# Performance work log

Hardware: AMD Instinct MI355X
Metric: run time of the kernel (lower is better)

## Reference

```python
import jax, jax.numpy as jnp
import numpy as np

LORA_ALPHA = 16.0

def setup_inputs() -> dict:
    key = jax.random.key(0)
    kx, kw, ka, kb, kbias = jax.random.split(key, 5)
    B_, S, D_in, D_out, R = 2, 4096, 4096, 4096, 16
    x = jax.random.normal(kx, (B_, S, D_in), dtype=jnp.float32)
    W = jax.random.normal(kw, (D_out, D_in), dtype=jnp.float32) * 0.02
    A = jax.random.normal(ka, (R, D_in), dtype=jnp.float32) * 0.02
    Bm = jax.random.normal(kb, (D_out, R), dtype=jnp.float32) * 0.02
    bias = jax.random.normal(kbias, (D_out,), dtype=jnp.float32) * 0.02
    return {"x": x, "W": W, "A": A, "B": Bm, "bias": bias}

def reference(x, W, A, B, bias):
    # y = x @ W.T + bias + (alpha/rank) * (x @ A.T) @ B.T   (dropout p=0)
    rank = A.shape[0]
    lora_scale = LORA_ALPHA / rank
    y = jnp.einsum('bsd,nd->bsn', x, W) + bias
    h = jnp.einsum('bsd,rd->bsr', x, A)          # [B,S,r] low-rank down-proj
    y = y + lora_scale * jnp.einsum('bsr,nr->bsn', h, B)
    return y
```

## Files before the change

### kernel.cpp

```cpp
#include <hip/hip_runtime.h>
#include <hip/hip_bf16.h>

typedef short bf16x8 __attribute__((ext_vector_type(8)));
typedef float f32x4 __attribute__((ext_vector_type(4)));
typedef unsigned short ushort8v __attribute__((ext_vector_type(8)));

__device__ __forceinline__ unsigned short f2bf(float f) {
  unsigned u = __builtin_bit_cast(unsigned, f);
  u += 0x7fffu + ((u >> 16) & 1u);
  return (unsigned short)(u >> 16);
}

__device__ __forceinline__ void gload_lds16(const unsigned short* g, unsigned short* l) {
  __builtin_amdgcn_global_load_lds((const __attribute__((address_space(1))) void*)g,
                                   (__attribute__((address_space(3))) void*)l, 16, 0, 0);
}

__global__ __launch_bounds__(256) void prep_kernel(const float* __restrict__ x,
                                                   const float* __restrict__ W,
                                                   const float* __restrict__ A,
                                                   const float* __restrict__ Bm,
                                                   unsigned short* __restrict__ xb,
                                                   unsigned short* __restrict__ wb,
                                                   float scale, int K, int R, int n8, int t8) {
  int i = blockIdx.x * 256 + threadIdx.x;
  if (i < n8) {
    const float4* p = (const float4*)x + (size_t)i * 2;
    float4 a = p[0], b = p[1];
    ushort8v v;
    v[0] = f2bf(a.x); v[1] = f2bf(a.y); v[2] = f2bf(a.z); v[3] = f2bf(a.w);
    v[4] = f2bf(b.x); v[5] = f2bf(b.y); v[6] = f2bf(b.z); v[7] = f2bf(b.w);
    *((ushort8v*)xb + i) = v;
    return;
  }
  int idx = i - n8;
  if (idx >= t8) return;
  int perRow = K >> 3;
  int n = idx / perRow;
  int d0 = (idx - n * perRow) << 3;
  const float4* wp = (const float4*)(W + (size_t)n * K + d0);
  float4 w0 = wp[0], w1 = wp[1];
  float acc[8] = {w0.x, w0.y, w0.z, w0.w, w1.x, w1.y, w1.z, w1.w};
#pragma unroll 4
  for (int r = 0; r < R; ++r) {
    float c = Bm[(size_t)n * R + r] * scale;
    const float4* ap = (const float4*)(A + (size_t)r * K + d0);
    float4 a0 = ap[0], a1 = ap[1];
    acc[0] += c * a0.x; acc[1] += c * a0.y; acc[2] += c * a0.z; acc[3] += c * a0.w;
    acc[4] += c * a1.x; acc[5] += c * a1.y; acc[6] += c * a1.z; acc[7] += c * a1.w;
  }
  ushort8v v;
#pragma unroll
  for (int j = 0; j < 8; ++j) v[j] = f2bf(acc[j]);
  *((ushort8v*)wb + idx) = v;
}

__global__ __launch_bounds__(256, 2) void gemm_bt_bias_mb(const unsigned short* __restrict__ Xb,
                                                          const unsigned short* __restrict__ Wb,
                                                          const float* __restrict__ bias,
                                                          float* __restrict__ C,
                                                          int M, int N, int K) {
  __shared__ __align__(16) char lds[49152];
  const int t = threadIdx.x;
  const int wave = t >> 6, lane = t & 63;
  const int fr = lane & 15, kc = lane >> 4;
  const int wr = wave >> 1, wc = wave & 1;

  const int NTn = N >> 7;
  const int nwg = gridDim.x;
  int bid = blockIdx.x;
  if ((nwg & 7) == 0) bid = (bid & 7) * (nwg >> 3) + (bid >> 3);
  const int tm = bid / NTn, tn = bid % NTn;
  const int m0 = tm << 8, n0 = tn << 7;

  const int srow = t >> 3;
  const int gch8 = ((t & 7) ^ (srow & 7)) << 3;
  const unsigned short* pa = Xb + (size_t)(m0 + srow) * K + gch8;
  const unsigned short* pb = Wb + (size_t)(n0 + srow) * K + gch8;

  const int swz = (fr & 7) << 4;
  int offA0[8], offB0[4];
#pragma unroll
  for (int m = 0; m < 8; ++m)
    offA0[m] = (wr * 128 + m * 16 + fr) * 128 + ((kc << 4) ^ swz);
#pragma unroll
  for (int n = 0; n < 4; ++n)
    offB0[n] = 32768 + (wc * 64 + n * 16 + fr) * 128 + ((kc << 4) ^ swz);

  f32x4 acc[8][4];
#pragma unroll
  for (int m = 0; m < 8; ++m)
#pragma unroll
    for (int n = 0; n < 4; ++n) acc[m][n] = (f32x4){0.f, 0.f, 0.f, 0.f};

  const size_t K32 = (size_t)32 * K;

  for (int k0 = 0; k0 < K; k0 += 64) {
#pragma unroll
    for (int j = 0; j < 8; ++j)
      gload_lds16(pa + (size_t)j * K32 + k0,
                  (unsigned short*)((char*)lds + j * 4096) + t * 8);
#pragma unroll
    for (int j = 0; j < 4; ++j)
      gload_lds16(pb + (size_t)j * K32 + k0,
                  (unsigned short*)((char*)lds + 32768 + j * 4096) + t * 8);
    __syncthreads();

    bf16x8 af[8], bf[4];
#pragma unroll
    for (int m = 0; m < 8; ++m) af[m] = *(const bf16x8*)((char*)lds + offA0[m]);
#pragma unroll
    for (int n = 0; n < 4; ++n) bf[n] = *(const bf16x8*)((char*)lds + offB0[n]);
#pragma unroll
    for (int m = 0; m < 8; ++m)
#pragma unroll
      for (int n = 0; n < 4; ++n)
        acc[m][n] = __builtin_amdgcn_mfma_f32_16x16x32_bf16(af[m], bf[n], acc[m][n], 0, 0, 0);
#pragma unroll
    for (int m = 0; m < 8; ++m) af[m] = *(const bf16x8*)((char*)lds + (offA0[m] ^ 64));
#pragma unroll
    for (int n = 0; n < 4; ++n) bf[n] = *(const bf16x8*)((char*)lds + (offB0[n] ^ 64));
#pragma unroll
    for (int m = 0; m < 8; ++m)
#pragma unroll
      for (int n = 0; n < 4; ++n)
        acc[m][n] = __builtin_amdgcn_mfma_f32_16x16x32_bf16(af[m], bf[n], acc[m][n], 0, 0, 0);

    __syncthreads();
  }

  const int crow = (lane >> 4) * 4;
  const int ccol = lane & 15;
#pragma unroll
  for (int n = 0; n < 4; ++n) {
    int col = n0 + wc * 64 + n * 16 + ccol;
    float bv = bias[col];
#pragma unroll
    for (int m = 0; m < 8; ++m) {
      int row = m0 + wr * 128 + m * 16 + crow;
      float* cp = C + (size_t)row * N + col;
#pragma unroll
      for (int r = 0; r < 4; ++r) cp[(size_t)r * N] = acc[m][n][r] + bv;
    }
  }
}

__global__ __launch_bounds__(256) void gemm_bt_bias(const unsigned short* __restrict__ Xb,
                                                    const unsigned short* __restrict__ Wb,
                                                    const float* __restrict__ bias,
                                                    float* __restrict__ C,
                                                    int M, int N, int K) {
  __shared__ unsigned short sA[128 * 32];
  __shared__ unsigned short sB[128 * 32];
  const int t = threadIdx.x;
  const int wave = t >> 6, lane = t & 63;
  const int NT = N >> 7;
  const int nwg = gridDim.x;
  int bid = blockIdx.x;
  if ((nwg & 7) == 0) bid = (bid & 7) * (nwg >> 3) + (bid >> 3);
  const int tm = bid / NT, tn = bid % NT;
  const int m0 = tm << 7, n0 = tn << 7;
  const int wr = wave >> 1, wc = wave & 1;

  f32x4 acc[4][4];
#pragma unroll
  for (int m = 0; m < 4; ++m)
#pragma unroll
    for (int n = 0; n < 4; ++n) acc[m][n] = (f32x4){0.f, 0.f, 0.f, 0.f};

  const unsigned short* gA0 = Xb + (size_t)(m0 + (t >> 2)) * K + (t & 3) * 8;
  const unsigned short* gA1 = Xb + (size_t)(m0 + 64 + (t >> 2)) * K + (t & 3) * 8;
  const unsigned short* gB0 = Wb + (size_t)(n0 + (t >> 2)) * K + (t & 3) * 8;
  const unsigned short* gB1 = Wb + (size_t)(n0 + 64 + (t >> 2)) * K + (t & 3) * 8;
  unsigned short* lA0 = sA + (size_t)(wave * 64) * 8;
  unsigned short* lA1 = sA + (size_t)(256 + wave * 64) * 8;
  unsigned short* lB0 = sB + (size_t)(wave * 64) * 8;
  unsigned short* lB1 = sB + (size_t)(256 + wave * 64) * 8;

  const int rrow = lane & 15;
  const int rk = (lane >> 4) * 8;

  for (int k0 = 0; k0 < K; k0 += 32) {
    gload_lds16(gA0 + k0, lA0);
    gload_lds16(gA1 + k0, lA1);
    gload_lds16(gB0 + k0, lB0);
    gload_lds16(gB1 + k0, lB1);
    __syncthreads();
    bf16x8 af[4], bfr[4];
#pragma unroll
    for (int m = 0; m < 4; ++m)
      af[m] = *(const bf16x8*)&sA[(size_t)(wr * 64 + m * 16 + rrow) * 32 + rk];
#pragma unroll
    for (int n = 0; n < 4; ++n)
      bfr[n] = *(const bf16x8*)&sB[(size_t)(wc * 64 + n * 16 + rrow) * 32 + rk];
#pragma unroll
    for (int m = 0; m < 4; ++m)
#pragma unroll
      for (int n = 0; n < 4; ++n)
        acc[m][n] = __builtin_amdgcn_mfma_f32_16x16x32_bf16(af[m], bfr[n], acc[m][n], 0, 0, 0);
    __syncthreads();
  }
  const int crow0 = (lane >> 4) * 4;
  const int ccol = lane & 15;
#pragma unroll
  for (int n = 0; n < 4; ++n) {
    int col = n0 + wc * 64 + n * 16 + ccol;
    float bv = bias[col];
#pragma unroll
    for (int m = 0; m < 4; ++m) {
      int row = m0 + wr * 64 + m * 16 + crow0;
      float* cp = C + (size_t)row * N + col;
#pragma unroll
      for (int r = 0; r < 4; ++r) cp[(size_t)r * N] = acc[m][n][r] + bv;
    }
  }
}

__global__ __launch_bounds__(64) void lora_h_kernel(const float* __restrict__ x,
                                                    const float* __restrict__ A,
                                                    float* __restrict__ h,
                                                    float scale, int K, int R) {
  int m = blockIdx.x, lane = threadIdx.x;
  float acc[16];
#pragma unroll
  for (int r = 0; r < 16; ++r) acc[r] = 0.f;
  for (int d = lane; d < K; d += 64) {
    float xv = x[(size_t)m * K + d];
    for (int r = 0; r < R; ++r) acc[r] += xv * A[(size_t)r * K + d];
  }
  for (int off = 32; off; off >>= 1)
    for (int r = 0; r < R; ++r) acc[r] += __shfl_down(acc[r], off);
  if (lane == 0)
    for (int r = 0; r < R; ++r) h[(size_t)m * R + r] = acc[r] * scale;
}

__global__ __launch_bounds__(256) void fgemm_fallback(const float* __restrict__ X,
                                                      const float* __restrict__ W,
                                                      const float* __restrict__ Bm,
                                                      const float* __restrict__ bias,
                                                      const float* __restrict__ h,
                                                      float* __restrict__ C,
                                                      int M, int N, int K, int R) {
  __shared__ float sX[64][20];
  __shared__ float sW[64][20];
  int nt = N >> 6;
  int bx = blockIdx.x % nt, by = blockIdx.x / nt;
  int m0 = by << 6, n0 = bx << 6;
  int t = threadIdx.x;
  int tx = t & 15, ty = t >> 4;
  float acc[4][4] = {};
  int lrr = t >> 2, lc = (t & 3) << 2;
  for (int k0 = 0; k0 < K; k0 += 16) {
    *(float4*)&sX[lrr][lc] = *(const float4*)&X[(size_t)(m0 + lrr) * K + k0 + lc];
    *(float4*)&sW[lrr][lc] = *(const float4*)&W[(size_t)(n0 + lrr) * K + k0 + lc];
    __syncthreads();
#pragma unroll
    for (int kk = 0; kk < 16; ++kk) {
      float a[4], b[4];
#pragma unroll
      for (int i = 0; i < 4; ++i) a[i] = sX[ty * 4 + i][kk];
#pragma unroll
      for (int j = 0; j < 4; ++j) b[j] = sW[tx * 4 + j][kk];
#pragma unroll
      for (int i = 0; i < 4; ++i)
#pragma unroll
        for (int j = 0; j < 4; ++j) acc[i][j] += a[i] * b[j];
    }
    __syncthreads();
  }
#pragma unroll
  for (int i = 0; i < 4; ++i) {
    int row = m0 + ty * 4 + i;
#pragma unroll
    for (int j = 0; j < 4; ++j) {
      int col = n0 + tx * 4 + j;
      float lo = 0.f;
      for (int r = 0; r < R; ++r) lo += h[(size_t)row * R + r] * Bm[(size_t)col * R + r];
      C[(size_t)row * N + col] = acc[i][j] + bias[col] + lo;
    }
  }
}

extern "C" void kernel_launch(void* const* d_in, const int* in_sizes, int n_in,
                              void* d_out, int out_size, void* d_ws, size_t ws_size,
                              hipStream_t stream) {
  const float* x    = (const float*)d_in[0];
  const float* W    = (const float*)d_in[1];
  const float* A    = (const float*)d_in[2];
  const float* Bm   = (const float*)d_in[3];
  const float* bias = (const float*)d_in[4];
  float* out = (float*)d_out;

  const int N = in_sizes[4];
  const int R = in_sizes[3] / N;
  const int K = in_sizes[2] / R;
  const int M = in_sizes[0] / K;
  const float scale = 16.0f / (float)R;

  const size_t xbytes = (size_t)M * K * 2;
  const size_t wbytes = (size_t)N * K * 2;
  const bool ws_ok = (ws_size >= xbytes + wbytes);
  const bool fastMB  = ws_ok && (M % 256 == 0) && (N % 128 == 0) && (K % 64 == 0) && (K >= 64);
  const bool fast128 = ws_ok && (M % 128 == 0) && (N % 128 == 0) && (K % 32 == 0);

  if (fastMB || fast128) {
    unsigned short* xb = (unsigned short*)d_ws;
    unsigned short* wb = (unsigned short*)((char*)d_ws + xbytes);
    int n8 = M * K / 8;
    int t8 = N * K / 8;
    int total = n8 + t8;
    prep_kernel<<<dim3((total + 255) / 256), dim3(256), 0, stream>>>(x, W, A, Bm, xb, wb,
                                                                     scale, K, R, n8, t8);
    if (fastMB) {
      int grid = (M / 256) * (N / 128);
      gemm_bt_bias_mb<<<dim3(grid), dim3(256), 0, stream>>>(xb, wb, bias, out, M, N, K);
    } else {
      int grid = (M / 128) * (N / 128);
      gemm_bt_bias<<<dim3(grid), dim3(256), 0, stream>>>(xb, wb, bias, out, M, N, K);
    }
  } else {
    float* h = (float*)d_ws;
    lora_h_kernel<<<dim3(M), dim3(64), 0, stream>>>(x, A, h, scale, K, R);
    int grid = (M / 64) * (N / 64);
    fgemm_fallback<<<dim3(grid), dim3(256), 0, stream>>>(x, W, Bm, bias, h, out, M, N, K, R);
  }
}
```

Baseline: 354.8 us.

## Replace 256x128 GEMM with double-buffered 256x256 tile and staged prefetch pipeline

Replaces the single-buffered 256x128 bf16 GEMM with a 256x256 tile that double-buffers K-slices in 128 KB of LDS. Global-to-LDS loads for the next slice are issued in quarters, interleaved with four MFMA quadrant phases under explicit vmcnt waits, barriers and raised wave priority. This targets the exposed load latency of the old per-iteration sync loop and raises arithmetic intensity per loaded byte. The cost is one workgroup per CU, very high register pressure from a 64-entry accumulator array, and a grid of only 256 blocks, which may fill the CUs unevenly.

After: 460.2 us. 1.3x slower.

```diff
diff --git a/kernel.cpp b/kernel.cpp
--- a/kernel.cpp
+++ b/kernel.cpp
@@ -4,6 +4,10 @@
 typedef short bf16x8 __attribute__((ext_vector_type(8)));
 typedef float f32x4 __attribute__((ext_vector_type(4)));
 typedef unsigned short ushort8v __attribute__((ext_vector_type(8)));
+
+#define SBAR() asm volatile("s_barrier" ::: "memory")
+#define SB0() __builtin_amdgcn_sched_barrier(0)
+#define LGKM0() do { asm volatile("s_waitcnt lgkmcnt(0)" ::: "memory"); SB0(); } while (0)
 
 __device__ __forceinline__ unsigned short f2bf(float f) {
   unsigned u = __builtin_bit_cast(unsigned, f);
@@ -55,94 +59,151 @@
   *((ushort8v*)wb + idx) = v;
 }
 
-__global__ __launch_bounds__(256, 2) void gemm_bt_bias_mb(const unsigned short* __restrict__ Xb,
-                                                          const unsigned short* __restrict__ Wb,
-                                                          const float* __restrict__ bias,
-                                                          float* __restrict__ C,
-                                                          int M, int N, int K) {
-  __shared__ __align__(16) char lds[49152];
+__global__ __launch_bounds__(256, 1) void gemm256x4_bt_bias(const unsigned short* __restrict__ Xb,
+                                                            const unsigned short* __restrict__ Wb,
+                                                            const float* __restrict__ bias,
+                                                            float* __restrict__ C,
+                                                            int M, int N, int K) {
+  __shared__ __align__(16) char lds[131072];
   const int t = threadIdx.x;
   const int wave = t >> 6, lane = t & 63;
   const int fr = lane & 15, kc = lane >> 4;
   const int wr = wave >> 1, wc = wave & 1;
 
-  const int NTn = N >> 7;
+  const int NTn = N >> 8;
   const int nwg = gridDim.x;
   int bid = blockIdx.x;
   if ((nwg & 7) == 0) bid = (bid & 7) * (nwg >> 3) + (bid >> 3);
   const int tm = bid / NTn, tn = bid % NTn;
-  const int m0 = tm << 8, n0 = tn << 7;
-
-  const int srow = t >> 3;
-  const int gch8 = ((t & 7) ^ (srow & 7)) << 3;
-  const unsigned short* pa = Xb + (size_t)(m0 + srow) * K + gch8;
-  const unsigned short* pb = Wb + (size_t)(n0 + srow) * K + gch8;
+  const int m0 = tm << 8, n0 = tn << 8;
+
+  const int grow = t >> 3;
+  const int gch8 = ((t & 7) ^ (grow & 7)) << 3;
+  const unsigned short* pa0 = Xb + (size_t)(m0 + grow) * K + gch8;
+  const unsigned short* pb0 = Wb + (size_t)(n0 + grow) * K + gch8;
+  const size_t K32 = (size_t)32 * K;
+  const int sdst = t * 16;
 
   const int swz = (fr & 7) << 4;
-  int offA0[8], offB0[4];
+  const int cb0 = (kc << 4) ^ swz;
+  const int cb1 = ((4 + kc) << 4) ^ swz;
+  const char* rA0[2] = { (char*)lds + wr * 8192 + fr * 128 + cb0,
+                         (char*)lds + 65536 + wr * 8192 + fr * 128 + cb0 };
+  const char* rA1[2] = { (char*)lds + wr * 8192 + fr * 128 + cb1,
+                         (char*)lds + 65536 + wr * 8192 + fr * 128 + cb1 };
+  const char* rB0[2] = { (char*)lds + 32768 + wc * 8192 + fr * 128 + cb0,
+                         (char*)lds + 98304 + wc * 8192 + fr * 128 + cb0 };
+  const char* rB1[2] = { (char*)lds + 32768 + wc * 8192 + fr * 128 + cb1,
+                         (char*)lds + 98304 + wc * 8192 + fr * 128 + cb1 };
+
+  f32x4 acc[8][8];
 #pragma unroll
   for (int m = 0; m < 8; ++m)
-    offA0[m] = (wr * 128 + m * 16 + fr) * 128 + ((kc << 4) ^ swz);
-#pragma unroll
-  for (int n = 0; n < 4; ++n)
-    offB0[n] = 32768 + (wc * 64 + n * 16 + fr) * 128 + ((kc << 4) ^ swz);
-
-  f32x4 acc[8][4];
-#pragma unroll
-  for (int m = 0; m < 8; ++m)
-#pragma unroll
-    for (int n = 0; n < 4; ++n) acc[m][n] = (f32x4){0.f, 0.f, 0.f, 0.f};
-
-  const size_t K32 = (size_t)32 * K;
-
-  for (int k0 = 0; k0 < K; k0 += 64) {
-#pragma unroll
-    for (int j = 0; j < 8; ++j)
-      gload_lds16(pa + (size_t)j * K32 + k0,
-                  (unsigned short*)((char*)lds + j * 4096) + t * 8);
-#pragma unroll
-    for (int j = 0; j < 4; ++j)
-      gload_lds16(pb + (size_t)j * K32 + k0,
-                  (unsigned short*)((char*)lds + 32768 + j * 4096) + t * 8);
-    __syncthreads();
-
-    bf16x8 af[8], bf[4];
-#pragma unroll
-    for (int m = 0; m < 8; ++m) af[m] = *(const bf16x8*)((char*)lds + offA0[m]);
-#pragma unroll
-    for (int n = 0; n < 4; ++n) bf[n] = *(const bf16x8*)((char*)lds + offB0[n]);
-#pragma unroll
-    for (int m = 0; m < 8; ++m)
-#pragma unroll
-      for (int n = 0; n < 4; ++n)
-        acc[m][n] = __builtin_amdgcn_mfma_f32_16x16x32_bf16(af[m], bf[n], acc[m][n], 0, 0, 0);
-#pragma unroll
-    for (int m = 0; m < 8; ++m) af[m] = *(const bf16x8*)((char*)lds + (offA0[m] ^ 64));
-#pragma unroll
-    for (int n = 0; n < 4; ++n) bf[n] = *(const bf16x8*)((char*)lds + (offB0[n] ^ 64));
-#pragma unroll
-    for (int m = 0; m < 8; ++m)
-#pragma unroll
-      for (int n = 0; n < 4; ++n)
-        acc[m][n] = __builtin_amdgcn_mfma_f32_16x16x32_bf16(af[m], bf[n], acc[m][n], 0, 0, 0);
-
-    __syncthreads();
-  }
+#pragma unroll
+    for (int n = 0; n < 8; ++n) acc[m][n] = (f32x4){0.f, 0.f, 0.f, 0.f};
+
+  bf16x8 aF[8], bF0[8], bF1[8];
+
+#define GL(PSRC, DOFF) gload_lds16((PSRC), (unsigned short*)((char*)lds + (DOFF) + sdst))
+#define STG_A01(BUF, COL) do { GL(pa0 + (COL), (BUF)*65536 + 0); \
+    GL(pa0 + K32 + (COL), (BUF)*65536 + 4096); \
+    GL(pa0 + 4*K32 + (COL), (BUF)*65536 + 8192); \
+    GL(pa0 + 5*K32 + (COL), (BUF)*65536 + 12288); } while (0)
+#define STG_A23(BUF, COL) do { GL(pa0 + 2*K32 + (COL), (BUF)*65536 + 16384); \
+    GL(pa0 + 3*K32 + (COL), (BUF)*65536 + 20480); \
+    GL(pa0 + 6*K32 + (COL), (BUF)*65536 + 24576); \
+    GL(pa0 + 7*K32 + (COL), (BUF)*65536 + 28672); } while (0)
+#define STG_B01(BUF, COL) do { GL(pb0 + (COL), (BUF)*65536 + 32768); \
+    GL(pb0 + K32 + (COL), (BUF)*65536 + 36864); \
+    GL(pb0 + 4*K32 + (COL), (BUF)*65536 + 40960); \
+    GL(pb0 + 5*K32 + (COL), (BUF)*65536 + 45056); } while (0)
+#define STG_B23(BUF, COL) do { GL(pb0 + 2*K32 + (COL), (BUF)*65536 + 49152); \
+    GL(pb0 + 3*K32 + (COL), (BUF)*65536 + 53248); \
+    GL(pb0 + 6*K32 + (COL), (BUF)*65536 + 57344); \
+    GL(pb0 + 7*K32 + (COL), (BUF)*65536 + 61440); } while (0)
+
+#define RD_A(BUF, QM) do { \
+    const char* p0_ = rA0[BUF] + (QM)*16384; const char* p1_ = rA1[BUF] + (QM)*16384; \
+    aF[0]=*(const bf16x8*)(p0_);      aF[1]=*(const bf16x8*)(p1_); \
+    aF[2]=*(const bf16x8*)(p0_+2048); aF[3]=*(const bf16x8*)(p1_+2048); \
+    aF[4]=*(const bf16x8*)(p0_+4096); aF[5]=*(const bf16x8*)(p1_+4096); \
+    aF[6]=*(const bf16x8*)(p0_+6144); aF[7]=*(const bf16x8*)(p1_+6144); } while (0)
+#define RD_B(BUF, QN, DST) do { \
+    const char* p0_ = rB0[BUF] + (QN)*16384; const char* p1_ = rB1[BUF] + (QN)*16384; \
+    DST[0]=*(const bf16x8*)(p0_);      DST[1]=*(const bf16x8*)(p1_); \
+    DST[2]=*(const bf16x8*)(p0_+2048); DST[3]=*(const bf16x8*)(p1_+2048); \
+    DST[4]=*(const bf16x8*)(p0_+4096); DST[5]=*(const bf16x8*)(p1_+4096); \
+    DST[6]=*(const bf16x8*)(p0_+6144); DST[7]=*(const bf16x8*)(p1_+6144); } while (0)
+
+#define MMQ(QM, QN, BF) do { \
+    __builtin_amdgcn_s_setprio(1); \
+    _Pragma("unroll") for (int ks = 0; ks < 2; ++ks) \
+    _Pragma("unroll") for (int mi = 0; mi < 4; ++mi) \
+    _Pragma("unroll") for (int ni = 0; ni < 4; ++ni) \
+      acc[(QM)*4+mi][(QN)*4+ni] = __builtin_amdgcn_mfma_f32_16x16x32_bf16( \
+          aF[mi*2+ks], BF[ni*2+ks], acc[(QM)*4+mi][(QN)*4+ni], 0, 0, 0); \
+    __builtin_amdgcn_s_setprio(0); } while (0)
+
+#define STEP(BUF, DOSTG, VM1, VM2, VM4) do { \
+     \
+    RD_A(BUF, 0); RD_B(BUF, 0, bF0); \
+    if (DOSTG) { STG_A01((BUF)^1, col); } \
+    asm volatile("s_waitcnt vmcnt(" VM1 ")" ::: "memory"); \
+    SBAR(); LGKM0(); MMQ(0, 0, bF0); SBAR(); \
+     \
+    RD_B(BUF, 1, bF1); \
+    if (DOSTG) { STG_B01((BUF)^1, col); } \
+    asm volatile("s_waitcnt vmcnt(" VM2 ")" ::: "memory"); \
+    SBAR(); LGKM0(); MMQ(0, 1, bF1); SBAR(); \
+     \
+    RD_A(BUF, 1); \
+    if (DOSTG) { STG_B23((BUF)^1, col); } \
+    SBAR(); LGKM0(); MMQ(1, 0, bF0); SBAR(); \
+     \
+    if (DOSTG) { STG_A23((BUF)^1, col); } \
+    asm volatile("s_waitcnt vmcnt(" VM4 ")" ::: "memory"); \
+    SB0(); \
+    SBAR(); MMQ(1, 1, bF1); SBAR(); \
+    if (DOSTG) col += 64; \
+  } while (0)
+
+  size_t col = 0;
+  STG_A01(0, 0); STG_B01(0, 0); STG_B23(0, 0); STG_A23(0, 0);
+  asm volatile("s_waitcnt vmcnt(8)" ::: "memory");
+  SBAR();
+  col = 64;
+
+  const int NS = K >> 6;
+  for (int s2 = 0; s2 < NS - 2; s2 += 2) {
+    STEP(0, 1, "8", "8", "4");
+    STEP(1, 1, "8", "8", "4");
+  }
+  STEP(0, 1, "8", "8", "4");
+  STEP(1, 0, "4", "0", "0");
 
   const int crow = (lane >> 4) * 4;
   const int ccol = lane & 15;
 #pragma unroll
-  for (int n = 0; n < 4; ++n) {
-    int col = n0 + wc * 64 + n * 16 + ccol;
-    float bv = bias[col];
-#pragma unroll
-    for (int m = 0; m < 8; ++m) {
-      int row = m0 + wr * 128 + m * 16 + crow;
-      float* cp = C + (size_t)row * N + col;
-#pragma unroll
-      for (int r = 0; r < 4; ++r) cp[(size_t)r * N] = acc[m][n][r] + bv;
-    }
-  }
+  for (int ni = 0; ni < 8; ++ni) {
+    int colI = n0 + wc * 128 + ni * 16 + ccol;
+    float bv = bias[colI];
+#pragma unroll
+    for (int mi = 0; mi < 8; ++mi) {
+      int row = m0 + wr * 128 + mi * 16 + crow;
+      float* cp = C + (size_t)row * N + colI;
+#pragma unroll
+      for (int r = 0; r < 4; ++r) cp[(size_t)r * N] = acc[mi][ni][r] + bv;
+    }
+  }
+#undef GL
+#undef STG_A01
+#undef STG_A23
+#undef STG_B01
+#undef STG_B23
+#undef RD_A
+#undef RD_B
+#undef MMQ
+#undef STEP
 }
 
 __global__ __launch_bounds__(256) void gemm_bt_bias(const unsigned short* __restrict__ Xb,
@@ -300,10 +361,10 @@
   const size_t xbytes = (size_t)M * K * 2;
   const size_t wbytes = (size_t)N * K * 2;
   const bool ws_ok = (ws_size >= xbytes + wbytes);
-  const bool fastMB  = ws_ok && (M % 256 == 0) && (N % 128 == 0) && (K % 64 == 0) && (K >= 64);
+  const bool fast256 = ws_ok && (M % 256 == 0) && (N % 256 == 0) && (K % 128 == 0) && (K >= 256);
   const bool fast128 = ws_ok && (M % 128 == 0) && (N % 128 == 0) && (K % 32 == 0);
 
-  if (fastMB || fast128) {
+  if (fast256 || fast128) {
     unsigned short* xb = (unsigned short*)d_ws;
     unsigned short* wb = (unsigned short*)((char*)d_ws + xbytes);
     int n8 = M * K / 8;
@@ -311,9 +372,9 @@
     int total = n8 + t8;
     prep_kernel<<<dim3((total + 255) / 256), dim3(256), 0, stream>>>(x, W, A, Bm, xb, wb,
                                                                      scale, K, R, n8, t8);
-    if (fastMB) {
-      int grid = (M / 256) * (N / 128);
-      gemm_bt_bias_mb<<<dim3(grid), dim3(256), 0, stream>>>(xb, wb, bias, out, M, N, K);
+    if (fast256) {
+      int grid = (M / 256) * (N / 256);
+      gemm256x4_bt_bias<<<dim3(grid), dim3(256), 0, stream>>>(xb, wb, bias, out, M, N, K);
     } else {
       int grid = (M / 128) * (N / 128);
       gemm_bt_bias<<<dim3(grid), dim3(256), 0, stream>>>(xb, wb, bias, out, M, N, K);
```

## Rewrite main GEMM as double-buffered 128x128 tile with interleaved direct-to-LDS loads

Applied to the files above, without the earlier changes.

Replaces the single-buffered 256x128 GEMM with a 128x128 tile kernel that double-buffers LDS (64KB) and splits each K-step into four quarters. Global-to-LDS loads for the next stage are interleaved with MFMA work, gated by explicit vmcnt/lgkmcnt waits and raw s_barrier, with s_setprio raised around the MFMA bursts. The goal is to hide global-load latency behind compute instead of stalling on a barrier every K-step. The smaller tile doubles the grid and lowers per-tile reuse, and the larger LDS footprint may limit occupancy.

After: 374.0 us. 1.05x slower.

```diff
diff --git a/kernel.cpp b/kernel.cpp
--- a/kernel.cpp
+++ b/kernel.cpp
@@ -4,6 +4,10 @@
 typedef short bf16x8 __attribute__((ext_vector_type(8)));
 typedef float f32x4 __attribute__((ext_vector_type(4)));
 typedef unsigned short ushort8v __attribute__((ext_vector_type(8)));
+
+#define SBAR() asm volatile("s_barrier" ::: "memory")
+#define SB0() __builtin_amdgcn_sched_barrier(0)
+#define LGKM0() do { asm volatile("s_waitcnt lgkmcnt(0)" ::: "memory"); SB0(); } while (0)
 
 __device__ __forceinline__ unsigned short f2bf(float f) {
   unsigned u = __builtin_bit_cast(unsigned, f);
@@ -55,12 +59,12 @@
   *((ushort8v*)wb + idx) = v;
 }
 
-__global__ __launch_bounds__(256, 2) void gemm_bt_bias_mb(const unsigned short* __restrict__ Xb,
-                                                          const unsigned short* __restrict__ Wb,
-                                                          const float* __restrict__ bias,
-                                                          float* __restrict__ C,
-                                                          int M, int N, int K) {
-  __shared__ __align__(16) char lds[49152];
+__global__ __launch_bounds__(256, 2) void gemm128mb_bt_bias(const unsigned short* __restrict__ Xb,
+                                                            const unsigned short* __restrict__ Wb,
+                                                            const float* __restrict__ bias,
+                                                            float* __restrict__ C,
+                                                            int M, int N, int K) {
+  __shared__ __align__(16) char lds[65536];
   const int t = threadIdx.x;
   const int wave = t >> 6, lane = t & 63;
   const int fr = lane & 15, kc = lane >> 4;
@@ -71,78 +75,114 @@
   int bid = blockIdx.x;
   if ((nwg & 7) == 0) bid = (bid & 7) * (nwg >> 3) + (bid >> 3);
   const int tm = bid / NTn, tn = bid % NTn;
-  const int m0 = tm << 8, n0 = tn << 7;
+  const int m0 = tm << 7, n0 = tn << 7;
 
   const int srow = t >> 3;
   const int gch8 = ((t & 7) ^ (srow & 7)) << 3;
-  const unsigned short* pa = Xb + (size_t)(m0 + srow) * K + gch8;
-  const unsigned short* pb = Wb + (size_t)(n0 + srow) * K + gch8;
+  const unsigned short* pa0 = Xb + (size_t)(m0 + srow) * K + gch8;
+  const unsigned short* pb0 = Wb + (size_t)(n0 + srow) * K + gch8;
+  const size_t K32 = (size_t)32 * K;
+  const int sdst = t * 16;
 
   const int swz = (fr & 7) << 4;
-  int offA0[8], offB0[4];
-#pragma unroll
-  for (int m = 0; m < 8; ++m)
-    offA0[m] = (wr * 128 + m * 16 + fr) * 128 + ((kc << 4) ^ swz);
-#pragma unroll
-  for (int n = 0; n < 4; ++n)
-    offB0[n] = 32768 + (wc * 64 + n * 16 + fr) * 128 + ((kc << 4) ^ swz);
-
-  f32x4 acc[8][4];
-#pragma unroll
-  for (int m = 0; m < 8; ++m)
+  const int cb0 = (kc << 4) ^ swz;
+  const int cb1 = ((4 + kc) << 4) ^ swz;
+  const char* rA0[2] = { (char*)lds + (wr * 64 + fr) * 128 + cb0,
+                         (char*)lds + 32768 + (wr * 64 + fr) * 128 + cb0 };
+  const char* rA1[2] = { (char*)lds + (wr * 64 + fr) * 128 + cb1,
+                         (char*)lds + 32768 + (wr * 64 + fr) * 128 + cb1 };
+  const char* rB0[2] = { (char*)lds + 16384 + (wc * 64 + fr) * 128 + cb0,
+                         (char*)lds + 49152 + (wc * 64 + fr) * 128 + cb0 };
+  const char* rB1[2] = { (char*)lds + 16384 + (wc * 64 + fr) * 128 + cb1,
+                         (char*)lds + 49152 + (wc * 64 + fr) * 128 + cb1 };
+
+  f32x4 acc[4][4];
+#pragma unroll
+  for (int m = 0; m < 4; ++m)
 #pragma unroll
     for (int n = 0; n < 4; ++n) acc[m][n] = (f32x4){0.f, 0.f, 0.f, 0.f};
 
-  const size_t K32 = (size_t)32 * K;
-
-  for (int k0 = 0; k0 < K; k0 += 64) {
-#pragma unroll
-    for (int j = 0; j < 8; ++j)
-      gload_lds16(pa + (size_t)j * K32 + k0,
-                  (unsigned short*)((char*)lds + j * 4096) + t * 8);
-#pragma unroll
-    for (int j = 0; j < 4; ++j)
-      gload_lds16(pb + (size_t)j * K32 + k0,
-                  (unsigned short*)((char*)lds + 32768 + j * 4096) + t * 8);
-    __syncthreads();
-
-    bf16x8 af[8], bf[4];
-#pragma unroll
-    for (int m = 0; m < 8; ++m) af[m] = *(const bf16x8*)((char*)lds + offA0[m]);
-#pragma unroll
-    for (int n = 0; n < 4; ++n) bf[n] = *(const bf16x8*)((char*)lds + offB0[n]);
-#pragma unroll
-    for (int m = 0; m < 8; ++m)
-#pragma unroll
-      for (int n = 0; n < 4; ++n)
-        acc[m][n] = __builtin_amdgcn_mfma_f32_16x16x32_bf16(af[m], bf[n], acc[m][n], 0, 0, 0);
-#pragma unroll
-    for (int m = 0; m < 8; ++m) af[m] = *(const bf16x8*)((char*)lds + (offA0[m] ^ 64));
-#pragma unroll
-    for (int n = 0; n < 4; ++n) bf[n] = *(const bf16x8*)((char*)lds + (offB0[n] ^ 64));
-#pragma unroll
-    for (int m = 0; m < 8; ++m)
-#pragma unroll
-      for (int n = 0; n < 4; ++n)
-        acc[m][n] = __builtin_amdgcn_mfma_f32_16x16x32_bf16(af[m], bf[n], acc[m][n], 0, 0, 0);
-
-    __syncthreads();
-  }
+  bf16x8 aQ[2], bQ[8];
+
+#define GL(PSRC, DOFF) gload_lds16((PSRC), (unsigned short*)((char*)lds + (DOFF) + sdst))
+#define STG_A(BUF, s, COL) GL(pa0 + (size_t)(s) * K32 + (COL), (BUF) * 32768 + (s) * 4096)
+#define STG_B(BUF, s, COL) GL(pb0 + (size_t)(s) * K32 + (COL), (BUF) * 32768 + 16384 + (s) * 4096)
+
+#define RD_B(BUF) do { \
+    bQ[0]=*(const bf16x8*)(rB0[BUF]);        bQ[1]=*(const bf16x8*)(rB1[BUF]); \
+    bQ[2]=*(const bf16x8*)(rB0[BUF]+2048);   bQ[3]=*(const bf16x8*)(rB1[BUF]+2048); \
+    bQ[4]=*(const bf16x8*)(rB0[BUF]+4096);   bQ[5]=*(const bf16x8*)(rB1[BUF]+4096); \
+    bQ[6]=*(const bf16x8*)(rB0[BUF]+6144);   bQ[7]=*(const bf16x8*)(rB1[BUF]+6144); } while (0)
+#define RD_A(BUF, mq) do { \
+    aQ[0]=*(const bf16x8*)(rA0[BUF]+(mq)*2048); \
+    aQ[1]=*(const bf16x8*)(rA1[BUF]+(mq)*2048); } while (0)
+
+#define MMQ(mq) do { __builtin_amdgcn_s_setprio(1); \
+    _Pragma("unroll") for (int nf = 0; nf < 4; ++nf) \
+    _Pragma("unroll") for (int ks = 0; ks < 2; ++ks) \
+      acc[mq][nf] = __builtin_amdgcn_mfma_f32_16x16x32_bf16( \
+          aQ[ks], bQ[nf*2+ks], acc[mq][nf], 0, 0, 0); \
+    __builtin_amdgcn_s_setprio(0); } while (0)
+
+#define STEP(BUF, DOSTG, VM2, VM4) do { \
+     \
+    RD_B(BUF); RD_A(BUF, 0); \
+    if (DOSTG) { STG_A(BUF^1, 0, col); STG_A(BUF^1, 2, col); } \
+    SBAR(); LGKM0(); MMQ(0); SBAR(); \
+     \
+    RD_A(BUF, 1); \
+    if (DOSTG) { STG_B(BUF^1, 0, col); STG_B(BUF^1, 1, col); } \
+    asm volatile("s_waitcnt vmcnt(" VM2 ")" ::: "memory"); \
+    SBAR(); LGKM0(); MMQ(1); SBAR(); \
+     \
+    RD_A(BUF, 2); \
+    if (DOSTG) { STG_B(BUF^1, 2, col); STG_B(BUF^1, 3, col); } \
+    SBAR(); LGKM0(); MMQ(2); SBAR(); \
+     \
+    RD_A(BUF, 3); \
+    if (DOSTG) { STG_A(BUF^1, 1, col); STG_A(BUF^1, 3, col); } \
+    asm volatile("s_waitcnt vmcnt(" VM4 ")" ::: "memory"); \
+    SBAR(); LGKM0(); MMQ(3); SBAR(); \
+    if (DOSTG) col += 64; \
+  } while (0)
+
+  size_t col = 0;
+  STG_A(0, 0, 0); STG_A(0, 2, 0);
+  STG_B(0, 0, 0); STG_B(0, 1, 0); STG_B(0, 2, 0); STG_B(0, 3, 0);
+  STG_A(0, 1, 0); STG_A(0, 3, 0);
+  asm volatile("s_waitcnt vmcnt(2)" ::: "memory");
+  SBAR();
+  col = 64;
+
+  const int NT = K >> 6;
+  for (int s2 = 0; s2 < NT - 2; s2 += 2) {
+    STEP(0, 1, "4", "2");
+    STEP(1, 1, "4", "2");
+  }
+  STEP(0, 1, "4", "2");
+  STEP(1, 0, "0", "0");
 
   const int crow = (lane >> 4) * 4;
   const int ccol = lane & 15;
 #pragma unroll
   for (int n = 0; n < 4; ++n) {
-    int col = n0 + wc * 64 + n * 16 + ccol;
-    float bv = bias[col];
-#pragma unroll
-    for (int m = 0; m < 8; ++m) {
-      int row = m0 + wr * 128 + m * 16 + crow;
-      float* cp = C + (size_t)row * N + col;
+    int colI = n0 + wc * 64 + n * 16 + ccol;
+    float bv = bias[colI];
+#pragma unroll
+    for (int m = 0; m < 4; ++m) {
+      int row = m0 + wr * 64 + m * 16 + crow;
+      float* cp = C + (size_t)row * N + colI;
 #pragma unroll
       for (int r = 0; r < 4; ++r) cp[(size_t)r * N] = acc[m][n][r] + bv;
     }
   }
+#undef GL
+#undef STG_A
+#undef STG_B
+#undef RD_B
+#undef RD_A
+#undef MMQ
+#undef STEP
 }
 
 __global__ __launch_bounds__(256) void gemm_bt_bias(const unsigned short* __restrict__ Xb,
@@ -300,7 +340,7 @@
   const size_t xbytes = (size_t)M * K * 2;
   const size_t wbytes = (size_t)N * K * 2;
   const bool ws_ok = (ws_size >= xbytes + wbytes);
-  const bool fastMB  = ws_ok && (M % 256 == 0) && (N % 128 == 0) && (K % 64 == 0) && (K >= 64);
+  const bool fastMB  = ws_ok && (M % 128 == 0) && (N % 128 == 0) && (K % 128 == 0) && (K >= 256);
   const bool fast128 = ws_ok && (M % 128 == 0) && (N % 128 == 0) && (K % 32 == 0);
 
   if (fastMB || fast128) {
@@ -312,8 +352,8 @@
     prep_kernel<<<dim3((total + 255) / 256), dim3(256), 0, stream>>>(x, W, A, Bm, xb, wb,
                                                                      scale, K, R, n8, t8);
     if (fastMB) {
-      int grid = (M / 256) * (N / 128);
-      gemm_bt_bias_mb<<<dim3(grid), dim3(256), 0, stream>>>(xb, wb, bias, out, M, N, K);
+      int grid = (M / 128) * (N / 128);
+      gemm128mb_bt_bias<<<dim3(grid), dim3(256), 0, stream>>>(xb, wb, bias, out, M, N, K);
     } else {
       int grid = (M / 128) * (N / 128);
       gemm_bt_bias<<<dim3(grid), dim3(256), 0, stream>>>(xb, wb, bias, out, M, N, K);
```
